# Kernel tuning notes

Hardware: AMD Instinct MI355X
Metric: run time of the kernel (lower is better)

The kernel has to match this reference:

```python
import jax, jax.numpy as jnp
import numpy as np

TEMPERATURE = 0.07
BASE_TEMPERATURE = 0.07
L_MAX = 16  # max number of session labels per dialogue
NEG_INF = -1e30


def setup_inputs() -> dict:
    key = jax.random.key(0)
    k1, k2, k3 = jax.random.split(key, 3)
    B, T, H = 128, 1024, 256
    features = jax.random.normal(k1, (B, T, H), dtype=jnp.float32)
    dialogue_lengths = jax.random.randint(k2, (B,), 1, T + 1)
    labels = jax.random.randint(k3, (B, T), 0, L_MAX)
    return {"features": features, "dialogue_lengths": dialogue_lengths, "labels": labels}


def reference(features, dialogue_lengths, labels):
    B, T, H = features.shape
    valid = jnp.arange(T)[None, :] < dialogue_lengths[:, None]            # [B,T]
    # one-hot label assignment, zeroed at padded positions
    oh = (labels[..., None] == jnp.arange(L_MAX)[None, None, :]) & valid[..., None]
    ohf = oh.astype(features.dtype)                                       # [B,T,L]
    counts = ohf.sum(axis=1)                                              # [B,L]
    # per-dialogue, per-label prototype = mean of member features
    proto_sum = jnp.einsum('btl,bth->blh', ohf, features)                 # [B,L,H]
    prototypes = proto_sum / jnp.maximum(counts, 1.0)[..., None]          # [B,L,H]
    # anchor-vs-prototype logits
    logits = jnp.einsum('bth,blh->btl', features, prototypes) / TEMPERATURE
    present = counts > 0                                                  # [B,L]
    logits = jnp.where(present[:, None, :], logits, NEG_INF)
    log_prob = jax.nn.log_softmax(logits, axis=-1)                        # [B,T,L]
    # mask is one-hot on each token's own label -> mean_log_prob_pos is log_prob at own label
    pos = jnp.take_along_axis(log_prob, labels[..., None], axis=-1)[..., 0]  # [B,T]
    tok_loss = -(TEMPERATURE / BASE_TEMPERATURE) * pos
    per_dialogue = jnp.sum(jnp.where(valid, tok_loss, 0.0), axis=1) / dialogue_lengths.astype(features.dtype)
    return per_dialogue.mean()
```

## Files before the change

### kernel.cpp

```cpp
#include <hip/hip_runtime.h>
#include <math.h>

#define B 128
#define T 1024
#define H 256
#define L 16
#define INV_TEMP (1.0f/0.07f)
#define NEG_INF -1e30f


__global__ __launch_bounds__(256) void proto_kernel(
    const float* __restrict__ feat, const int* __restrict__ dlen,
    const int* __restrict__ labels, float* __restrict__ ws_pp,
    int* __restrict__ ws_cntp) {
  __shared__ float acc[4][L * 128];
  __shared__ int labs[256];
  __shared__ int cnt[L];

  const int bx = blockIdx.x;
  const int b = bx >> 3;
  const int chunk = (bx >> 2) & 1;
  const int seg = bx & 3;
  const int tid = threadIdx.x;
  const int w = tid >> 6;
  const int lane = tid & 63;

  const int len = dlen[b];
  if (seg * 256 >= len) return;

  for (int i = tid; i < 4 * L * 128; i += 256) ((float*)acc)[i] = 0.f;
  labs[tid] = labels[(size_t)b * T + seg * 256 + tid];
  if (tid < L) cnt[tid] = 0;
  __syncthreads();

  if (chunk == 0 && (seg * 256 + tid) < len) atomicAdd(&cnt[labs[tid]], 1);

  int nt = len - seg * 256 - w * 64;
  if (nt > 64) nt = 64;
  const float2* fbase = (const float2*)(feat +
      ((size_t)b * T + seg * 256 + w * 64) * H + chunk * 128);
  float* a = acc[w];

  int j = 0;
  for (; j + 4 <= nt; j += 4) {
    float2 f0 = fbase[(size_t)(j + 0) * (H / 2) + lane];
    float2 f1 = fbase[(size_t)(j + 1) * (H / 2) + lane];
    float2 f2 = fbase[(size_t)(j + 2) * (H / 2) + lane];
    float2 f3 = fbase[(size_t)(j + 3) * (H / 2) + lane];
    const int l0 = labs[w * 64 + j + 0];
    const int l1 = labs[w * 64 + j + 1];
    const int l2 = labs[w * 64 + j + 2];
    const int l3 = labs[w * 64 + j + 3];
    float2* p0 = (float2*)&a[l0 * 128 + lane * 2];
    { float2 v = *p0; v.x += f0.x; v.y += f0.y; *p0 = v; }
    float2* p1 = (float2*)&a[l1 * 128 + lane * 2];
    { float2 v = *p1; v.x += f1.x; v.y += f1.y; *p1 = v; }
    float2* p2 = (float2*)&a[l2 * 128 + lane * 2];
    { float2 v = *p2; v.x += f2.x; v.y += f2.y; *p2 = v; }
    float2* p3 = (float2*)&a[l3 * 128 + lane * 2];
    { float2 v = *p3; v.x += f3.x; v.y += f3.y; *p3 = v; }
  }
  for (; j < nt; ++j) {
    float2 f = fbase[(size_t)j * (H / 2) + lane];
    const int lab = labs[w * 64 + j];
    float2* p = (float2*)&a[lab * 128 + lane * 2];
    float2 v = *p; v.x += f.x; v.y += f.y; *p = v;
  }
  __syncthreads();

  float* op = ws_pp + (((size_t)b * 4 + seg) * L) * H + chunk * 128;
  for (int e = tid; e < L * 128; e += 256) {
    const float s = acc[0][e] + acc[1][e] + acc[2][e] + acc[3][e];
    op[(e >> 7) * H + (e & 127)] = s;
  }
  if (chunk == 0 && tid < L) ws_cntp[(b * 4 + seg) * L + tid] = cnt[tid];
}

__global__ __launch_bounds__(256) void dots_kernel(
    const float* __restrict__ feat, const int* __restrict__ dlen,
    const float* __restrict__ ws_pp, const int* __restrict__ ws_cntp,
    float* __restrict__ ws_dots) {
  __shared__ float pr[L * 128];
  __shared__ int cnts[L];

  const int bx = blockIdx.x;
  const int b = bx >> 1;
  const int half = bx & 1;
  const int tid = threadIdx.x;

  const int len = dlen[b];
  const int nseg = (len + 255) >> 8;

  if (tid < L) {
    const int* cp = ws_cntp + b * 4 * L + tid;
    int c = 0;
    for (int s = 0; s < nseg; ++s) c += cp[s * L];
    cnts[tid] = c;
  }
  __syncthreads();

  const float* gp = ws_pp + ((size_t)b * 4 * L) * H + half * 128;
  for (int i = tid; i < L * 128; i += 256) {
    const int l = i >> 7, c = i & 127;
    float s = 0.f;
    for (int sg = 0; sg < nseg; ++sg) s += gp[(sg * L + l) * H + c];
    const int cn = cnts[l];
    pr[i] = s * (cn > 0 ? 1.f / (float)cn : 0.f);
  }
  __syncthreads();

  const float4* fv[4];
#pragma unroll
  for (int k = 0; k < 4; ++k) {
    const int t = k * 256 + tid;
    fv[k] = (const float4*)(feat + ((size_t)b * T + t) * H + half * 128);
  }

  float dot[4][L];
#pragma unroll
  for (int k = 0; k < 4; ++k)
#pragma unroll
    for (int l = 0; l < L; ++l) dot[k][l] = 0.f;

  for (int cb = 0; cb < 8; ++cb) {
    float4 f[4][4];
#pragma unroll
    for (int k = 0; k < 4; ++k) {
      if (k < nseg) {
#pragma unroll
        for (int q = 0; q < 4; ++q) f[k][q] = fv[k][cb * 4 + q];
      }
    }
#pragma unroll
    for (int q = 0; q < 4; ++q) {
#pragma unroll
      for (int l = 0; l < L; ++l) {
        const float4 p = *(const float4*)&pr[l * 128 + cb * 16 + q * 4];
#pragma unroll
        for (int k = 0; k < 4; ++k) {
          if (k < nseg) {
            dot[k][l] += f[k][q].x * p.x + f[k][q].y * p.y +
                         f[k][q].z * p.z + f[k][q].w * p.w;
          }
        }
      }
    }
  }

#pragma unroll
  for (int k = 0; k < 4; ++k) {
    const int t = k * 256 + tid;
    if (k < nseg && t < len) {
      float4* d = (float4*)(ws_dots + (((size_t)half * B + b) * T + t) * L);
#pragma unroll
      for (int q = 0; q < 4; ++q)
        d[q] = make_float4(dot[k][q * 4], dot[k][q * 4 + 1],
                           dot[k][q * 4 + 2], dot[k][q * 4 + 3]);
    }
  }
}

__global__ __launch_bounds__(256) void loss_kernel(
    const int* __restrict__ dlen, const int* __restrict__ labels,
    const int* __restrict__ ws_cntp, const float* __restrict__ ws_dots,
    float* __restrict__ out) {
  __shared__ int cnts[L];
  __shared__ float red[256];

  const int b = blockIdx.x >> 2;
  const int seg = blockIdx.x & 3;
  const int tid = threadIdx.x;

  const int len = dlen[b];
  if (seg * 256 >= len) return;
  const int nseg = (len + 255) >> 8;

  if (tid < L) {
    const int* cp = ws_cntp + b * 4 * L + tid;
    int c = 0;
    for (int s = 0; s < nseg; ++s) c += cp[s * L];
    cnts[tid] = c;
  }
  __syncthreads();

  const int t = seg * 256 + tid;
  float tok = 0.f;

  if (t < len) {
    const float* d0 = ws_dots + ((size_t)b * T + t) * L;
    const float* d1 = d0 + (size_t)B * T * L;
    float lg[L];
#pragma unroll
    for (int l = 0; l < L; ++l) {
      const float d = d0[l] + d1[l];
      lg[l] = (cnts[l] > 0) ? d * INV_TEMP : NEG_INF;
    }
    float m = lg[0];
#pragma unroll
    for (int l = 1; l < L; ++l) m = fmaxf(m, lg[l]);
    float se = 0.f;
#pragma unroll
    for (int l = 0; l < L; ++l) se += expf(lg[l] - m);
    const float lsp = m + logf(se);

    const int lab = labels[(size_t)b * T + t];
    float pos = 0.f;
#pragma unroll
    for (int l = 0; l < L; ++l) pos += (l == lab) ? lg[l] : 0.f;

    tok = lsp - pos;
  }

  red[tid] = tok;
  __syncthreads();
#pragma unroll
  for (int s = 128; s > 0; s >>= 1) {
    if (tid < s) red[tid] += red[tid + s];
    __syncthreads();
  }
  if (tid == 0) atomicAdd(out, red[0] / ((float)len * (float)B));
}

extern "C" void kernel_launch(void* const* d_in, const int* in_sizes, int n_in,
                              void* d_out, int out_size, void* d_ws, size_t ws_size,
                              hipStream_t stream) {
  const float* feat = (const float*)d_in[0];
  const int* dlen = (const int*)d_in[1];
  const int* labels = (const int*)d_in[2];
  float* out = (float*)d_out;

  float* ws_pp = (float*)d_ws;
  int* ws_cntp = (int*)(ws_pp + (size_t)B * 4 * L * H);
  float* ws_dots = (float*)(ws_cntp + (size_t)B * 4 * L);

  hipMemsetAsync(out, 0, sizeof(float), stream);
  proto_kernel<<<B * 8, 256, 0, stream>>>(feat, dlen, labels, ws_pp, ws_cntp);
  dots_kernel<<<B * 2, 256, 0, stream>>>(feat, dlen, ws_pp, ws_cntp, ws_dots);
  loss_kernel<<<B * 4, 256, 0, stream>>>(dlen, labels, ws_cntp, ws_dots, out);
}
```

Baseline: 232.2 us.

## Fuse dots and loss kernels, zero output inside proto kernel

Merges the prototype-dot kernel and the log-softmax loss kernel into one kernel where each thread computes all 16 dot products over the full hidden dimension for its own token and then the loss. This removes the ws_dots round trip through global memory and one launch, and the memset is replaced by a store in the first proto block. Each block now rebuilds the full 16x256 prototype tile in shared memory, and each thread reads a whole 1 KB feature row uncoalesced. The grid for the dot work changes from 256 to 512 blocks. Zeroing the output inside proto_kernel relies on stream ordering before the later atomics.

```diff
diff --git a/kernel.cpp b/kernel.cpp
--- a/kernel.cpp
+++ b/kernel.cpp
@@ -12,12 +12,14 @@
 __global__ __launch_bounds__(256) void proto_kernel(
     const float* __restrict__ feat, const int* __restrict__ dlen,
     const int* __restrict__ labels, float* __restrict__ ws_pp,
-    int* __restrict__ ws_cntp) {
+    int* __restrict__ ws_cntp, float* __restrict__ out) {
   __shared__ float acc[4][L * 128];
   __shared__ int labs[256];
   __shared__ int cnt[L];
 
   const int bx = blockIdx.x;
+  if (bx == 0 && threadIdx.x == 0) out[0] = 0.f;
+
   const int b = bx >> 3;
   const int chunk = (bx >> 2) & 1;
   const int seg = bx & 3;
@@ -76,94 +78,11 @@
   if (chunk == 0 && tid < L) ws_cntp[(b * 4 + seg) * L + tid] = cnt[tid];
 }
 
-__global__ __launch_bounds__(256) void dots_kernel(
+__global__ __launch_bounds__(256) void dotsloss_kernel(
     const float* __restrict__ feat, const int* __restrict__ dlen,
-    const float* __restrict__ ws_pp, const int* __restrict__ ws_cntp,
-    float* __restrict__ ws_dots) {
-  __shared__ float pr[L * 128];
-  __shared__ int cnts[L];
-
-  const int bx = blockIdx.x;
-  const int b = bx >> 1;
-  const int half = bx & 1;
-  const int tid = threadIdx.x;
-
-  const int len = dlen[b];
-  const int nseg = (len + 255) >> 8;
-
-  if (tid < L) {
-    const int* cp = ws_cntp + b * 4 * L + tid;
-    int c = 0;
-    for (int s = 0; s < nseg; ++s) c += cp[s * L];
-    cnts[tid] = c;
-  }
-  __syncthreads();
-
-  const float* gp = ws_pp + ((size_t)b * 4 * L) * H + half * 128;
-  for (int i = tid; i < L * 128; i += 256) {
-    const int l = i >> 7, c = i & 127;
-    float s = 0.f;
-    for (int sg = 0; sg < nseg; ++sg) s += gp[(sg * L + l) * H + c];
-    const int cn = cnts[l];
-    pr[i] = s * (cn > 0 ? 1.f / (float)cn : 0.f);
-  }
-  __syncthreads();
-
-  const float4* fv[4];
-#pragma unroll
-  for (int k = 0; k < 4; ++k) {
-    const int t = k * 256 + tid;
-    fv[k] = (const float4*)(feat + ((size_t)b * T + t) * H + half * 128);
-  }
-
-  float dot[4][L];
-#pragma unroll
-  for (int k = 0; k < 4; ++k)
-#pragma unroll
-    for (int l = 0; l < L; ++l) dot[k][l] = 0.f;
-
-  for (int cb = 0; cb < 8; ++cb) {
-    float4 f[4][4];
-#pragma unroll
-    for (int k = 0; k < 4; ++k) {
-      if (k < nseg) {
-#pragma unroll
-        for (int q = 0; q < 4; ++q) f[k][q] = fv[k][cb * 4 + q];
-      }
-    }
-#pragma unroll
-    for (int q = 0; q < 4; ++q) {
-#pragma unroll
-      for (int l = 0; l < L; ++l) {
-        const float4 p = *(const float4*)&pr[l * 128 + cb * 16 + q * 4];
-#pragma unroll
-        for (int k = 0; k < 4; ++k) {
-          if (k < nseg) {
-            dot[k][l] += f[k][q].x * p.x + f[k][q].y * p.y +
-                         f[k][q].z * p.z + f[k][q].w * p.w;
-          }
-        }
-      }
-    }
-  }
-
-#pragma unroll
-  for (int k = 0; k < 4; ++k) {
-    const int t = k * 256 + tid;
-    if (k < nseg && t < len) {
-      float4* d = (float4*)(ws_dots + (((size_t)half * B + b) * T + t) * L);
-#pragma unroll
-      for (int q = 0; q < 4; ++q)
-        d[q] = make_float4(dot[k][q * 4], dot[k][q * 4 + 1],
-                           dot[k][q * 4 + 2], dot[k][q * 4 + 3]);
-    }
-  }
-}
-
-__global__ __launch_bounds__(256) void loss_kernel(
-    const int* __restrict__ dlen, const int* __restrict__ labels,
-    const int* __restrict__ ws_cntp, const float* __restrict__ ws_dots,
-    float* __restrict__ out) {
+    const int* __restrict__ labels, const float* __restrict__ ws_pp,
+    const int* __restrict__ ws_cntp, float* __restrict__ out) {
+  __shared__ float pr[L * H];
   __shared__ int cnts[L];
   __shared__ float red[256];
 
@@ -183,18 +102,45 @@
   }
   __syncthreads();
 
+  const float* gp = ws_pp + (size_t)b * 4 * L * H;
+  for (int i = tid; i < L * H; i += 256) {
+    const int l = i >> 8;
+    float s = 0.f;
+    for (int sg = 0; sg < nseg; ++sg) s += gp[(sg * L + l) * H + (i & (H - 1))];
+    const int cn = cnts[l];
+    pr[i] = s * (cn > 0 ? 1.f / (float)cn : 0.f);
+  }
+  __syncthreads();
+
   const int t = seg * 256 + tid;
   float tok = 0.f;
 
   if (t < len) {
-    const float* d0 = ws_dots + ((size_t)b * T + t) * L;
-    const float* d1 = d0 + (size_t)B * T * L;
+    const float4* f4 = (const float4*)(feat + ((size_t)b * T + t) * H);
+    float dot[L];
+#pragma unroll
+    for (int l = 0; l < L; ++l) dot[l] = 0.f;
+
+#pragma unroll 4
+    for (int cb = 0; cb < 16; ++cb) {
+      float4 f[4];
+#pragma unroll
+      for (int q = 0; q < 4; ++q) f[q] = f4[cb * 4 + q];
+#pragma unroll
+      for (int q = 0; q < 4; ++q) {
+#pragma unroll
+        for (int l = 0; l < L; ++l) {
+          const float4 p = *(const float4*)&pr[l * H + cb * 16 + q * 4];
+          dot[l] += f[q].x * p.x + f[q].y * p.y +
+                    f[q].z * p.z + f[q].w * p.w;
+        }
+      }
+    }
+
     float lg[L];
 #pragma unroll
-    for (int l = 0; l < L; ++l) {
-      const float d = d0[l] + d1[l];
-      lg[l] = (cnts[l] > 0) ? d * INV_TEMP : NEG_INF;
-    }
+    for (int l = 0; l < L; ++l)
+      lg[l] = (cnts[l] > 0) ? dot[l] * INV_TEMP : NEG_INF;
     float m = lg[0];
 #pragma unroll
     for (int l = 1; l < L; ++l) m = fmaxf(m, lg[l]);
@@ -231,10 +177,7 @@
 
   float* ws_pp = (float*)d_ws;
   int* ws_cntp = (int*)(ws_pp + (size_t)B * 4 * L * H);
-  float* ws_dots = (float*)(ws_cntp + (size_t)B * 4 * L);
 
-  hipMemsetAsync(out, 0, sizeof(float), stream);
-  proto_kernel<<<B * 8, 256, 0, stream>>>(feat, dlen, labels, ws_pp, ws_cntp);
-  dots_kernel<<<B * 2, 256, 0, stream>>>(feat, dlen, ws_pp, ws_cntp, ws_dots);
-  loss_kernel<<<B * 4, 256, 0, stream>>>(dlen, labels, ws_cntp, ws_dots, out);
+  proto_kernel<<<B * 8, 256, 0, stream>>>(feat, dlen, labels, ws_pp, ws_cntp, out);
+  dotsloss_kernel<<<B * 4, 256, 0, stream>>>(feat, dlen, labels, ws_pp, ws_cntp, out);
 }
```

Measured after the change: 238.0 us. 1.02x slower.
